# Kernel optimization log

Measured on AMD Instinct MI355X. Metric: run time of the kernel, lower is better.

The kernel has to match this reference:

```python
import jax, jax.numpy as jnp
import numpy as np

N_NODES = 200_000   # total nodes in graph
N1 = 81_920         # layer-1 node set (union of sampled 1-hop neighbors)
B = 8_192           # batch of target nodes
S = 10              # neighbor fanout (num_sample=10 in the torch code)
F = 128             # raw feature dim (input_size)
D = 128             # out_size


def setup_inputs() -> dict:
    key = jax.random.key(0)
    ks = jax.random.split(key, 7)
    raw_features = jax.random.normal(ks[0], (N_NODES, F), dtype=jnp.float32)
    # xavier-ish scale for weights [out, 2*in]
    W1 = jax.random.normal(ks[1], (D, 2 * F), dtype=jnp.float32) * (1.0 / np.sqrt(2 * F))
    W2 = jax.random.normal(ks[2], (D, 2 * D), dtype=jnp.float32) * (1.0 / np.sqrt(2 * D))
    self_idx1 = jax.random.randint(ks[3], (N1,), 0, N_NODES)
    neigh_idx1 = jax.random.randint(ks[4], (N1, S), 0, N_NODES)
    self_idx2 = jax.random.randint(ks[5], (B,), 0, N1)
    neigh_idx2 = jax.random.randint(ks[6], (B, S), 0, N1)
    return {
        "raw_features": raw_features,
        "W1": W1,
        "W2": W2,
        "self_idx1": self_idx1,
        "neigh_idx1": neigh_idx1,
        "self_idx2": self_idx2,
        "neigh_idx2": neigh_idx2,
    }


def _sage_layer(self_feats, agg_feats, W):
    # torch: relu(W.mm(cat([self, agg], 1).t()).t()  == relu(cat @ W.T)
    combined = jnp.concatenate([self_feats, agg_feats], axis=1)
    return jax.nn.relu(combined @ W.T)


def reference(raw_features, W1, W2, self_idx1, neigh_idx1, self_idx2, neigh_idx2):
    # Layer 1: MEAN aggregate sampled neighbors from raw features (dense-mask
    # mean in torch == mean over sampled neighbor rows here), then Sage transform.
    agg1 = jnp.mean(raw_features[neigh_idx1], axis=1)          # [N1, F]
    h1 = _sage_layer(raw_features[self_idx1], agg1, W1)        # [N1, D]
    # Layer 2: aggregate over layer-1 embeddings (indices map into layer-1 rows,
    # mirroring _nodes_map / unique_nodes_dict in the torch code).
    agg2 = jnp.mean(h1[neigh_idx2], axis=1)                    # [B, D]
    out = _sage_layer(h1[self_idx2], agg2, W2)                 # [B, D]
    return out
```

## Files before the change

### kernel.cpp

```cpp
#include <hip/hip_runtime.h>
#include <hip/hip_bf16.h>

typedef __attribute__((ext_vector_type(4))) float f32x4;
typedef __attribute__((ext_vector_type(8))) short bf16x8;

__device__ __forceinline__ unsigned short f2bf(float f) {
    unsigned int u = __float_as_uint(f);
    u = (u + 0x7FFFu + ((u >> 16) & 1u)) >> 16;
    return (unsigned short)u;
}

__device__ __forceinline__ float bf2f(unsigned short u) {
    return __uint_as_float(((unsigned int)u) << 16);
}

__global__ __launch_bounds__(256) void cvt_fused(const float* __restrict__ feat,
                                                 const float* __restrict__ W1,
                                                 const float* __restrict__ W2,
                                                 unsigned short* __restrict__ featb,
                                                 unsigned short* __restrict__ W1b,
                                                 unsigned short* __restrict__ W2b) {
    if (blockIdx.x < 12500) {
        size_t i = ((size_t)blockIdx.x * 256 + threadIdx.x) * 8;
        float4 a = *(const float4*)(feat + i);
        float4 b = *(const float4*)(feat + i + 4);
        bf16x8 o;
        o[0] = (short)f2bf(a.x); o[1] = (short)f2bf(a.y);
        o[2] = (short)f2bf(a.z); o[3] = (short)f2bf(a.w);
        o[4] = (short)f2bf(b.x); o[5] = (short)f2bf(b.y);
        o[6] = (short)f2bf(b.z); o[7] = (short)f2bf(b.w);
        *(bf16x8*)(featb + i) = o;
    } else {
        int i = (blockIdx.x - 12500) * 256 + threadIdx.x;
        W1b[i] = f2bf(W1[i]);
        W2b[i] = f2bf(W2[i]);
    }
}

template<bool OUT_BF16>
__global__ __launch_bounds__(256, 4)
void sage_layer32(const unsigned short* __restrict__ src,
                  const unsigned short* __restrict__ Wb,
                  const int* __restrict__ self_idx,
                  const int* __restrict__ neigh_idx,
                  void* __restrict__ out_v) {
    __shared__ unsigned short As[32][264];
    __shared__ int sIdx[32];
    __shared__ int nIdx[320];

    const int t = threadIdx.x;
    const int rowBase = blockIdx.x * 32;

    if (t < 32) sIdx[t] = self_idx[rowBase + t];
    for (int i = t; i < 320; i += 256) nIdx[i] = neigh_idx[rowBase * 10 + i];
    __syncthreads();

    const int r0 = t >> 4;
    const int r1 = r0 + 16;
    const int co = (t & 15) * 8;

    bf16x8 sv0 = *(const bf16x8*)(src + (size_t)sIdx[r0] * 128 + co);
    bf16x8 sv1 = *(const bf16x8*)(src + (size_t)sIdx[r1] * 128 + co);
    bf16x8 nv0[10], nv1[10];
    #pragma unroll
    for (int sn = 0; sn < 10; ++sn)
        nv0[sn] = *(const bf16x8*)(src + (size_t)nIdx[r0 * 10 + sn] * 128 + co);
    #pragma unroll
    for (int sn = 0; sn < 10; ++sn)
        nv1[sn] = *(const bf16x8*)(src + (size_t)nIdx[r1 * 10 + sn] * 128 + co);

    *(bf16x8*)&As[r0][co] = sv0;
    *(bf16x8*)&As[r1][co] = sv1;

    float s0[8], s1[8];
    #pragma unroll
    for (int e = 0; e < 8; ++e) { s0[e] = 0.f; s1[e] = 0.f; }
    #pragma unroll
    for (int sn = 0; sn < 10; ++sn) {
        #pragma unroll
        for (int e = 0; e < 8; ++e) s0[e] += bf2f((unsigned short)nv0[sn][e]);
    }
    #pragma unroll
    for (int sn = 0; sn < 10; ++sn) {
        #pragma unroll
        for (int e = 0; e < 8; ++e) s1[e] += bf2f((unsigned short)nv1[sn][e]);
    }
    bf16x8 o0, o1;
    #pragma unroll
    for (int e = 0; e < 8; ++e) {
        o0[e] = (short)f2bf(s0[e] * 0.1f);
        o1[e] = (short)f2bf(s1[e] * 0.1f);
    }
    *(bf16x8*)&As[r0][128 + co] = o0;
    *(bf16x8*)&As[r1][128 + co] = o1;
    __syncthreads();

    const int lane = t & 63;
    const int w = t >> 6;
    const int rows16 = (w & 1) * 16;
    const int cols64 = (w >> 1) * 64;
    const int arow = rows16 + (lane & 15);
    const int ko = (lane >> 4) * 8;
    const int ncol = lane & 15;

    f32x4 acc[4];
    #pragma unroll
    for (int i = 0; i < 4; ++i) acc[i] = (f32x4){0.f, 0.f, 0.f, 0.f};

    #pragma unroll
    for (int kk = 0; kk < 8; ++kk) {
        bf16x8 af = *(const bf16x8*)&As[arow][kk * 32 + ko];
        #pragma unroll
        for (int ct = 0; ct < 4; ++ct) {
            const unsigned short* wp = Wb + (size_t)(cols64 + ct * 16 + ncol) * 256 + kk * 32 + ko;
            bf16x8 bf = *(const bf16x8*)wp;
            acc[ct] = __builtin_amdgcn_mfma_f32_16x16x32_bf16(af, bf, acc[ct], 0, 0, 0);
        }
    }

    const int mr = rowBase + rows16 + (lane >> 4) * 4;
    if (OUT_BF16) {
        unsigned short* out = (unsigned short*)out_v;
        #pragma unroll
        for (int ct = 0; ct < 4; ++ct) {
            #pragma unroll
            for (int r = 0; r < 4; ++r) {
                out[(size_t)(mr + r) * 128 + cols64 + ct * 16 + ncol] = f2bf(fmaxf(acc[ct][r], 0.f));
            }
        }
    } else {
        float* out = (float*)out_v;
        #pragma unroll
        for (int ct = 0; ct < 4; ++ct) {
            #pragma unroll
            for (int r = 0; r < 4; ++r) {
                out[(size_t)(mr + r) * 128 + cols64 + ct * 16 + ncol] = fmaxf(acc[ct][r], 0.f);
            }
        }
    }
}

template<bool SRC_BF16, bool OUT_BF16>
__global__ __launch_bounds__(256, 2)
void sage_layer(const void* __restrict__ src_v,
                const unsigned short* __restrict__ Wb,
                const int* __restrict__ self_idx,
                const int* __restrict__ neigh_idx,
                void* __restrict__ out_v) {
    __shared__ unsigned short As[64][264];
    __shared__ int sIdx[64];
    __shared__ int nIdx[64][10];

    const int t = threadIdx.x;
    const int rowBase = blockIdx.x * 64;

    if (t < 64) sIdx[t] = self_idx[rowBase + t];
    for (int i = t; i < 640; i += 256) nIdx[i / 10][i % 10] = neigh_idx[rowBase * 10 + i];
    __syncthreads();

    #pragma unroll
    for (int it = 0; it < 16; ++it) {
        int c = it * 256 + t;
        int row = c >> 6;
        int cc = c & 63;
        float4 v;
        if (cc < 32) {
            if constexpr (SRC_BF16) {
                ushort4 u = *(const ushort4*)((const unsigned short*)src_v + (size_t)sIdx[row] * 128 + cc * 4);
                v.x = bf2f(u.x); v.y = bf2f(u.y); v.z = bf2f(u.z); v.w = bf2f(u.w);
            } else {
                v = *(const float4*)((const float*)src_v + (size_t)sIdx[row] * 128 + cc * 4);
            }
        } else {
            int fo = (cc - 32) * 4;
            float sx = 0.f, sy = 0.f, sz = 0.f, sw = 0.f;
            #pragma unroll
            for (int sn = 0; sn < 10; ++sn) {
                float4 x;
                if constexpr (SRC_BF16) {
                    ushort4 u = *(const ushort4*)((const unsigned short*)src_v + (size_t)nIdx[row][sn] * 128 + fo);
                    x.x = bf2f(u.x); x.y = bf2f(u.y); x.z = bf2f(u.z); x.w = bf2f(u.w);
                } else {
                    x = *(const float4*)((const float*)src_v + (size_t)nIdx[row][sn] * 128 + fo);
                }
                sx += x.x; sy += x.y; sz += x.z; sw += x.w;
            }
            v.x = sx * 0.1f; v.y = sy * 0.1f; v.z = sz * 0.1f; v.w = sw * 0.1f;
        }
        ushort4 o;
        o.x = f2bf(v.x); o.y = f2bf(v.y); o.z = f2bf(v.z); o.w = f2bf(v.w);
        *(ushort4*)&As[row][cc * 4] = o;
    }
    __syncthreads();

    const int lane = t & 63;
    const int w = t >> 6;
    const int arow = w * 16 + (lane & 15);
    const int ko = (lane >> 4) * 8;
    const int ncol = lane & 15;

    f32x4 acc[8];
    #pragma unroll
    for (int i = 0; i < 8; ++i) acc[i] = (f32x4){0.f, 0.f, 0.f, 0.f};

    #pragma unroll
    for (int kk = 0; kk < 8; ++kk) {
        bf16x8 af = *(const bf16x8*)&As[arow][kk * 32 + ko];
        #pragma unroll
        for (int ct = 0; ct < 8; ++ct) {
            const unsigned short* wp = Wb + (ct * 16 + ncol) * 256 + kk * 32 + ko;
            bf16x8 bf = *(const bf16x8*)wp;
            acc[ct] = __builtin_amdgcn_mfma_f32_16x16x32_bf16(af, bf, acc[ct], 0, 0, 0);
        }
    }

    const int mr = rowBase + w * 16 + (lane >> 4) * 4;
    if (OUT_BF16) {
        unsigned short* out = (unsigned short*)out_v;
        #pragma unroll
        for (int ct = 0; ct < 8; ++ct) {
            #pragma unroll
            for (int r = 0; r < 4; ++r) {
                out[(size_t)(mr + r) * 128 + ct * 16 + ncol] = f2bf(fmaxf(acc[ct][r], 0.f));
            }
        }
    } else {
        float* out = (float*)out_v;
        #pragma unroll
        for (int ct = 0; ct < 8; ++ct) {
            #pragma unroll
            for (int r = 0; r < 4; ++r) {
                out[(size_t)(mr + r) * 128 + ct * 16 + ncol] = fmaxf(acc[ct][r], 0.f);
            }
        }
    }
}

extern "C" void kernel_launch(void* const* d_in, const int* in_sizes, int n_in,
                              void* d_out, int out_size, void* d_ws, size_t ws_size,
                              hipStream_t stream) {
    const float* raw   = (const float*)d_in[0];
    const float* W1    = (const float*)d_in[1];
    const float* W2    = (const float*)d_in[2];
    const int* self1   = (const int*)d_in[3];
    const int* neigh1  = (const int*)d_in[4];
    const int* self2   = (const int*)d_in[5];
    const int* neigh2  = (const int*)d_in[6];
    float* out = (float*)d_out;

    char* ws = (char*)d_ws;
    unsigned short* W1b  = (unsigned short*)ws;
    unsigned short* W2b  = W1b + 128 * 256;
    unsigned short* h1   = W2b + 128 * 256;
    unsigned short* rawb = h1 + (size_t)81920 * 128;
    const size_t need = (size_t)(128 * 256 * 2 + 81920 * 128 + (size_t)200000 * 128) * 2;

    if (ws_size >= need) {
        cvt_fused<<<12628, 256, 0, stream>>>(raw, W1, W2, rawb, W1b, W2b);
        sage_layer32<true><<<81920 / 32, 256, 0, stream>>>(
            rawb, W1b, self1, neigh1, (void*)h1);
        sage_layer32<false><<<8192 / 32, 256, 0, stream>>>(
            h1, W2b, self2, neigh2, (void*)out);
    } else {
        cvt_fused<<<12628, 256, 0, stream>>>(raw, W1, W2, rawb, W1b, W2b);
        sage_layer<false, true><<<81920 / 64, 256, 0, stream>>>(
            (const void*)raw, W1b, self1, neigh1, (void*)h1);
        sage_layer<true, false><<<8192 / 64, 256, 0, stream>>>(
            (const void*)h1, W2b, self2, neigh2, (void*)out);
    }
}
```

Measured before the change: 89.09 us.

## Gather neighbor rows via direct global-to-LDS loads with 16-row tiles

Replaces the register-based neighbor gather with buffer global_load_lds DMA copies into a shared staging area of 160 rows, then reduces the mean from LDS. The tile shrinks from 32 to 16 rows per block, and each wave now computes a 16x32 output slice. The aim is to cut VGPR pressure and keep more gather loads in flight. The cost is about 45KB of LDS per block, which limits occupancy, plus twice as many blocks and more redundant weight loads per output row.

```diff
diff --git a/kernel.cpp b/kernel.cpp
--- a/kernel.cpp
+++ b/kernel.cpp
@@ -3,6 +3,9 @@
 
 typedef __attribute__((ext_vector_type(4))) float f32x4;
 typedef __attribute__((ext_vector_type(8))) short bf16x8;
+
+#define AS1 __attribute__((address_space(1)))
+#define AS3 __attribute__((address_space(3)))
 
 __device__ __forceinline__ unsigned short f2bf(float f) {
     unsigned int u = __float_as_uint(f);
@@ -38,103 +41,97 @@
 }
 
 template<bool OUT_BF16>
-__global__ __launch_bounds__(256, 4)
-void sage_layer32(const unsigned short* __restrict__ src,
-                  const unsigned short* __restrict__ Wb,
-                  const int* __restrict__ self_idx,
-                  const int* __restrict__ neigh_idx,
-                  void* __restrict__ out_v) {
-    __shared__ unsigned short As[32][264];
-    __shared__ int sIdx[32];
-    __shared__ int nIdx[320];
+__global__ __launch_bounds__(256, 3)
+void sage_layer_dma(const unsigned short* __restrict__ src,
+                    const unsigned short* __restrict__ Wb,
+                    const int* __restrict__ self_idx,
+                    const int* __restrict__ neigh_idx,
+                    void* __restrict__ out_v) {
+    __shared__ unsigned short stage[160 * 128];
+    __shared__ unsigned short As[16][264];
 
     const int t = threadIdx.x;
-    const int rowBase = blockIdx.x * 32;
-
-    if (t < 32) sIdx[t] = self_idx[rowBase + t];
-    for (int i = t; i < 320; i += 256) nIdx[i] = neigh_idx[rowBase * 10 + i];
-    __syncthreads();
-
-    const int r0 = t >> 4;
-    const int r1 = r0 + 16;
-    const int co = (t & 15) * 8;
-
-    bf16x8 sv0 = *(const bf16x8*)(src + (size_t)sIdx[r0] * 128 + co);
-    bf16x8 sv1 = *(const bf16x8*)(src + (size_t)sIdx[r1] * 128 + co);
-    bf16x8 nv0[10], nv1[10];
-    #pragma unroll
-    for (int sn = 0; sn < 10; ++sn)
-        nv0[sn] = *(const bf16x8*)(src + (size_t)nIdx[r0 * 10 + sn] * 128 + co);
-    #pragma unroll
-    for (int sn = 0; sn < 10; ++sn)
-        nv1[sn] = *(const bf16x8*)(src + (size_t)nIdx[r1 * 10 + sn] * 128 + co);
-
-    *(bf16x8*)&As[r0][co] = sv0;
-    *(bf16x8*)&As[r1][co] = sv1;
-
-    float s0[8], s1[8];
-    #pragma unroll
-    for (int e = 0; e < 8; ++e) { s0[e] = 0.f; s1[e] = 0.f; }
-    #pragma unroll
-    for (int sn = 0; sn < 10; ++sn) {
-        #pragma unroll
-        for (int e = 0; e < 8; ++e) s0[e] += bf2f((unsigned short)nv0[sn][e]);
-    }
-    #pragma unroll
-    for (int sn = 0; sn < 10; ++sn) {
-        #pragma unroll
-        for (int e = 0; e < 8; ++e) s1[e] += bf2f((unsigned short)nv1[sn][e]);
-    }
-    bf16x8 o0, o1;
-    #pragma unroll
-    for (int e = 0; e < 8; ++e) {
-        o0[e] = (short)f2bf(s0[e] * 0.1f);
-        o1[e] = (short)f2bf(s1[e] * 0.1f);
-    }
-    *(bf16x8*)&As[r0][128 + co] = o0;
-    *(bf16x8*)&As[r1][128 + co] = o1;
-    __syncthreads();
-
     const int lane = t & 63;
     const int w = t >> 6;
-    const int rows16 = (w & 1) * 16;
-    const int cols64 = (w >> 1) * 64;
-    const int arow = rows16 + (lane & 15);
+    const int rowBase = blockIdx.x * 16;
+
+    const int w10 = w * 10;
+    int nri[10];
+    #pragma unroll
+    for (int li = 0; li < 10; ++li)
+        nri[li] = neigh_idx[rowBase * 10 + (w10 + li) * 4 + (lane >> 4)];
+
+    const int sr = self_idx[rowBase + (t >> 4)];
+    bf16x8 selfv = *(const bf16x8*)(src + (size_t)sr * 128 + (t & 15) * 8);
+
+    #pragma unroll
+    for (int li = 0; li < 10; ++li) {
+        const int i = w10 + li;
+        const unsigned short* gp = src + (size_t)nri[li] * 128 + (lane & 15) * 8;
+        unsigned short* lp = &stage[i * 512];
+        __builtin_amdgcn_global_load_lds((const AS1 void*)gp, (AS3 void*)lp, 16, 0, 0);
+    }
+
+    asm volatile("s_waitcnt vmcnt(0)" ::: "memory");
+    __syncthreads();
+
+    {
+        const int r = t >> 4;
+        const int co = (t & 15) * 8;
+        float s[8];
+        #pragma unroll
+        for (int e = 0; e < 8; ++e) s[e] = 0.f;
+        #pragma unroll
+        for (int j = 0; j < 10; ++j) {
+            bf16x8 v = *(const bf16x8*)&stage[(r * 10 + j) * 128 + co];
+            #pragma unroll
+            for (int e = 0; e < 8; ++e) s[e] += bf2f((unsigned short)v[e]);
+        }
+        bf16x8 o;
+        #pragma unroll
+        for (int e = 0; e < 8; ++e) o[e] = (short)f2bf(s[e] * 0.1f);
+        *(bf16x8*)&As[r][co] = selfv;
+        *(bf16x8*)&As[r][128 + co] = o;
+    }
+    __syncthreads();
+
+    const int cols32 = w * 32;
+    const int arow = lane & 15;
     const int ko = (lane >> 4) * 8;
     const int ncol = lane & 15;
 
-    f32x4 acc[4];
-    #pragma unroll
-    for (int i = 0; i < 4; ++i) acc[i] = (f32x4){0.f, 0.f, 0.f, 0.f};
+    f32x4 acc[2];
+    acc[0] = (f32x4){0.f, 0.f, 0.f, 0.f};
+    acc[1] = (f32x4){0.f, 0.f, 0.f, 0.f};
 
     #pragma unroll
     for (int kk = 0; kk < 8; ++kk) {
         bf16x8 af = *(const bf16x8*)&As[arow][kk * 32 + ko];
         #pragma unroll
-        for (int ct = 0; ct < 4; ++ct) {
-            const unsigned short* wp = Wb + (size_t)(cols64 + ct * 16 + ncol) * 256 + kk * 32 + ko;
+        for (int ct = 0; ct < 2; ++ct) {
+            const unsigned short* wp = Wb + (size_t)(cols32 + ct * 16 + ncol) * 256 + kk * 32 + ko;
             bf16x8 bf = *(const bf16x8*)wp;
             acc[ct] = __builtin_amdgcn_mfma_f32_16x16x32_bf16(af, bf, acc[ct], 0, 0, 0);
         }
     }
 
-    const int mr = rowBase + rows16 + (lane >> 4) * 4;
+    const int mr = rowBase + (lane >> 4) * 4;
     if (OUT_BF16) {
         unsigned short* out = (unsigned short*)out_v;
         #pragma unroll
-        for (int ct = 0; ct < 4; ++ct) {
-            #pragma unroll
-            for (int r = 0; r < 4; ++r) {
-                out[(size_t)(mr + r) * 128 + cols64 + ct * 16 + ncol] = f2bf(fmaxf(acc[ct][r], 0.f));
+        for (int ct = 0; ct < 2; ++ct) {
+            #pragma unroll
+            for (int r = 0; r < 4; ++r) {
+                out[(size_t)(mr + r) * 128 + cols32 + ct * 16 + ncol] = f2bf(fmaxf(acc[ct][r], 0.f));
             }
         }
     } else {
         float* out = (float*)out_v;
         #pragma unroll
-        for (int ct = 0; ct < 4; ++ct) {
-            #pragma unroll
-            for (int r = 0; r < 4; ++r) {
-                out[(size_t)(mr + r) * 128 + cols64 + ct * 16 + ncol] = fmaxf(acc[ct][r], 0.f);
+        for (int ct = 0; ct < 2; ++ct) {
+            #pragma unroll
+            for (int r = 0; r < 4; ++r) {
+                out[(size_t)(mr + r) * 128 + cols32 + ct * 16 + ncol] = fmaxf(acc[ct][r], 0.f);
             }
         }
     }
@@ -255,14 +252,14 @@
     unsigned short* rawb = h1 + (size_t)81920 * 128;
     const size_t need = (size_t)(128 * 256 * 2 + 81920 * 128 + (size_t)200000 * 128) * 2;
 
+    cvt_fused<<<12628, 256, 0, stream>>>(raw, W1, W2, rawb, W1b, W2b);
+
     if (ws_size >= need) {
-        cvt_fused<<<12628, 256, 0, stream>>>(raw, W1, W2, rawb, W1b, W2b);
-        sage_layer32<true><<<81920 / 32, 256, 0, stream>>>(
+        sage_layer_dma<true><<<81920 / 16, 256, 0, stream>>>(
             rawb, W1b, self1, neigh1, (void*)h1);
-        sage_layer32<false><<<8192 / 32, 256, 0, stream>>>(
+        sage_layer_dma<false><<<8192 / 16, 256, 0, stream>>>(
             h1, W2b, self2, neigh2, (void*)out);
     } else {
-        cvt_fused<<<12628, 256, 0, stream>>>(raw, W1, W2, rawb, W1b, W2b);
         sage_layer<false, true><<<81920 / 64, 256, 0, stream>>>(
             (const void*)raw, W1b, self1, neigh1, (void*)h1);
         sage_layer<true, false><<<8192 / 64, 256, 0, stream>>>(
```

New measurement: 93.81 us. 1.05x slower.
